# Kernel optimization log

Measured on AMD Instinct MI355X. Metric: run time of the kernel, lower is better.

The kernel has to match this reference:

```python
import jax, jax.numpy as jnp
import numpy as np

N_NODES = 100000

def _sage_conv(x, src, dst, Wl, bl, Wr, n_nodes):
    # PyG SAGEConv (mean aggr): out = lin_l(mean_{j in N(i)} x_j) + lin_r(x_i)
    msgs = x[src]                                            # [E, d] gather
    agg = jax.ops.segment_sum(msgs, dst, num_segments=n_nodes)   # [N, d]
    cnt = jax.ops.segment_sum(jnp.ones((src.shape[0],), x.dtype), dst,
                              num_segments=n_nodes)          # [N]
    mean = agg / jnp.maximum(cnt, 1.0)[:, None]              # mean aggregation
    return mean @ Wl.T + bl + x @ Wr.T

def setup_inputs() -> dict:
    key = jax.random.key(0)
    ks = jax.random.split(key, 6)
    d_in, d_hid, d_out = 64, 64, 2
    n_edges = 1600000
    x = jax.random.normal(ks[0], (N_NODES, d_in), dtype=jnp.float32)
    edge_index = jax.random.randint(ks[1], (2, n_edges), 0, N_NODES, dtype=jnp.int64)
    s = 1.0 / np.sqrt(d_in)
    W1l = jax.random.uniform(ks[2], (d_hid, d_in), jnp.float32, -s, s)
    b1l = jnp.zeros((d_hid,), jnp.float32)
    W1r = jax.random.uniform(ks[3], (d_hid, d_in), jnp.float32, -s, s)
    s2 = 1.0 / np.sqrt(d_hid)
    W2l = jax.random.uniform(ks[4], (d_out, d_hid), jnp.float32, -s2, s2)
    b2l = jnp.zeros((d_out,), jnp.float32)
    W2r = jax.random.uniform(ks[5], (d_out, d_hid), jnp.float32, -s2, s2)
    return {"x": x, "edge_index": edge_index, "W1l": W1l, "b1l": b1l,
            "W1r": W1r, "W2l": W2l, "b2l": b2l, "W2r": W2r}

def reference(x, edge_index, W1l, b1l, W1r, W2l, b2l, W2r):
    src, dst = edge_index[0], edge_index[1]
    h = _sage_conv(x, src, dst, W1l, b1l, W1r, N_NODES)
    h = jax.nn.relu(h)
    # F.dropout(p=0.5, training=False) is identity at inference
    out = _sage_conv(h, src, dst, W2l, b2l, W2r, N_NODES)
    return out
```

## Files before the change

### kernel.cpp

```cpp
#include <hip/hip_runtime.h>
#include <cstdint>

typedef long long i64;
typedef unsigned int u32;


#define BKT_SHIFT 8
#define BKT_MAX   512
#define BKT_CAP   5120
#define CHUNK     2048

__global__ __launch_bounds__(256) void k_detect(const int* __restrict__ e, int* __restrict__ flag) {
  __shared__ int nz;
  if (threadIdx.x == 0) nz = 0;
  __syncthreads();
  if (e[2 * threadIdx.x + 1] != 0) nz = 1;
  __syncthreads();
  if (threadIdx.x == 0) *flag = (nz == 0) ? 1 : 0;
}

__device__ __forceinline__ int edge_at(const void* eidx, int is64, size_t i) {
  return is64 ? (int)((const i64*)eidx)[i] : ((const int*)eidx)[i];
}

__global__ __launch_bounds__(256) void k_bucket(const void* __restrict__ eidx, const int* __restrict__ flag,
                                                int* __restrict__ gcount, u32* __restrict__ pairs, int E) {
  __shared__ int hist[BKT_MAX];
  __shared__ int basech[BKT_MAX];
  __shared__ int run[BKT_MAX];
  for (int i = threadIdx.x; i < BKT_MAX; i += 256) { hist[i] = 0; run[i] = 0; }
  __syncthreads();
  int is64 = *flag;
  int cbase = blockIdx.x * CHUNK;
  int cend = min(cbase + CHUNK, E);
  for (int e = cbase + threadIdx.x; e < cend; e += 256) {
    int d = edge_at(eidx, is64, (size_t)E + e);
    atomicAdd(&hist[d >> BKT_SHIFT], 1);
  }
  __syncthreads();
  for (int i = threadIdx.x; i < BKT_MAX; i += 256) {
    int h = hist[i];
    basech[i] = h ? (i * BKT_CAP + atomicAdd(&gcount[i], h)) : 0;
  }
  __syncthreads();
  for (int e = cbase + threadIdx.x; e < cend; e += 256) {
    int s = edge_at(eidx, is64, (size_t)e);
    int d = edge_at(eidx, is64, (size_t)E + e);
    int b = d >> BKT_SHIFT;
    int r = atomicAdd(&run[b], 1);
    pairs[basech[b] + r] = ((u32)s << 8) | (u32)(d & 255);
  }
}

__global__ __launch_bounds__(256) void k_csr(const int* __restrict__ gcount, const u32* __restrict__ pairs,
                                             int* __restrict__ csr_src, int* __restrict__ rs,
                                             int* __restrict__ re, int n_nodes) {
  __shared__ int cnt[256];
  __shared__ int sc[256];
  __shared__ int cur[256];
  int b = blockIdx.x, t = threadIdx.x;
  cnt[t] = 0;
  __syncthreads();
  int lo = b * BKT_CAP, hi = lo + gcount[b];
  for (int i = lo + t; i < hi; i += 256)
    atomicAdd(&cnt[pairs[i] & 255], 1);
  __syncthreads();
  int v = cnt[t];
  sc[t] = v;
  __syncthreads();
  for (int off = 1; off < 256; off <<= 1) {
    int a = (t >= off) ? sc[t - off] : 0;
    __syncthreads();
    sc[t] += a;
    __syncthreads();
  }
  int start = lo + sc[t] - v;
  int node = (b << BKT_SHIFT) + t;
  if (node < n_nodes) { rs[node] = start; re[node] = start + v; }
  cur[t] = start;
  __syncthreads();
  for (int i = lo + t; i < hi; i += 256) {
    u32 p = pairs[i];
    int q = atomicAdd(&cur[p & 255], 1);
    csr_src[q] = (int)(p >> 8);
  }
}

__global__ __launch_bounds__(256) void k_gemm1(const float* __restrict__ x,
                                               const float* __restrict__ Wl, const float* __restrict__ bl,
                                               const float* __restrict__ Wr,
                                               float* __restrict__ XL, float* __restrict__ XR, int n_nodes) {
  __shared__ float sWl[64 * 68];
  __shared__ float sWr[64 * 68];
  __shared__ float sX[64 * 68];
  int tid = threadIdx.x;
  int base = blockIdx.x * 64;

#pragma unroll
  for (int r = 0; r < 4; ++r) {
    int idx = tid + 256 * r;
    int f = idx >> 4, c4 = idx & 15;
    float4 wl = *(const float4*)(Wl + f * 64 + c4 * 4);
    float4 wr = *(const float4*)(Wr + f * 64 + c4 * 4);
    sWl[(c4 * 4 + 0) * 68 + f] = wl.x; sWl[(c4 * 4 + 1) * 68 + f] = wl.y;
    sWl[(c4 * 4 + 2) * 68 + f] = wl.z; sWl[(c4 * 4 + 3) * 68 + f] = wl.w;
    sWr[(c4 * 4 + 0) * 68 + f] = wr.x; sWr[(c4 * 4 + 1) * 68 + f] = wr.y;
    sWr[(c4 * 4 + 2) * 68 + f] = wr.z; sWr[(c4 * 4 + 3) * 68 + f] = wr.w;
  }
#pragma unroll
  for (int r = 0; r < 4; ++r) {
    int idx = tid + 256 * r;
    int nn = idx >> 4, c4 = idx & 15;
    int node = base + nn;
    float4 xv = make_float4(0.f, 0.f, 0.f, 0.f);
    if (node < n_nodes) xv = *(const float4*)(x + (size_t)node * 64 + c4 * 4);
    sX[(c4 * 4 + 0) * 68 + nn] = xv.x; sX[(c4 * 4 + 1) * 68 + nn] = xv.y;
    sX[(c4 * 4 + 2) * 68 + nn] = xv.z; sX[(c4 * 4 + 3) * 68 + nn] = xv.w;
  }
  __syncthreads();

  int f0 = (tid & 15) * 4, n0 = (tid >> 4) * 4;
  float accL[4][4] = {{0}}, accR[4][4] = {{0}};
#pragma unroll 8
  for (int k = 0; k < 64; ++k) {
    float4 xv = *(const float4*)&sX[k * 68 + n0];
    float4 wl = *(const float4*)&sWl[k * 68 + f0];
    float4 wr = *(const float4*)&sWr[k * 68 + f0];
    float xn[4] = {xv.x, xv.y, xv.z, xv.w};
    float wlf[4] = {wl.x, wl.y, wl.z, wl.w};
    float wrf[4] = {wr.x, wr.y, wr.z, wr.w};
#pragma unroll
    for (int a = 0; a < 4; ++a)
#pragma unroll
      for (int b = 0; b < 4; ++b) {
        accL[a][b] += xn[a] * wlf[b];
        accR[a][b] += xn[a] * wrf[b];
      }
  }

  float4 blv = *(const float4*)(bl + f0);
#pragma unroll
  for (int a = 0; a < 4; ++a) {
    int node = base + n0 + a;
    if (node >= n_nodes) continue;
    float4 ol = make_float4(accL[a][0], accL[a][1], accL[a][2], accL[a][3]);
    float4 orr = make_float4(accR[a][0] + blv.x, accR[a][1] + blv.y,
                             accR[a][2] + blv.z, accR[a][3] + blv.w);
    *(float4*)(XL + (size_t)node * 64 + f0) = ol;
    *(float4*)(XR + (size_t)node * 64 + f0) = orr;
  }
}

__global__ __launch_bounds__(256) void k_agg1g2(const int* __restrict__ rs, const int* __restrict__ re,
                                                const int* __restrict__ csr_src,
                                                const float* __restrict__ XL, const float* __restrict__ XR,
                                                const float* __restrict__ W2l, const float* __restrict__ b2l,
                                                const float* __restrict__ W2r,
                                                float* __restrict__ HL, float* __restrict__ HR,
                                                int n_nodes) {
  int wave = threadIdx.x >> 6, lane = threadIdx.x & 63;
  int g = lane >> 4, c = lane & 15;
  int n = (blockIdx.x * 4 + wave) * 4 + g;
  if (n >= n_nodes) return;

  float4 wl0 = *(const float4*)(W2l + c * 4);
  float4 wl1 = *(const float4*)(W2l + 64 + c * 4);
  float4 wr0 = *(const float4*)(W2r + c * 4);
  float4 wr1 = *(const float4*)(W2r + 64 + c * 4);
  float4 xr = *(const float4*)(XR + (size_t)n * 64 + c * 4);

  int start = rs[n], end = re[n];
  float4 a0 = make_float4(0.f, 0.f, 0.f, 0.f);
  float4 a1 = make_float4(0.f, 0.f, 0.f, 0.f);
  float4 a2 = make_float4(0.f, 0.f, 0.f, 0.f);
  float4 a3 = make_float4(0.f, 0.f, 0.f, 0.f);
  int e = start;
  for (; e + 3 < end; e += 4) {
    int s0 = csr_src[e], s1 = csr_src[e + 1], s2 = csr_src[e + 2], s3 = csr_src[e + 3];
    float4 v0 = *(const float4*)(XL + (size_t)s0 * 64 + c * 4);
    float4 v1 = *(const float4*)(XL + (size_t)s1 * 64 + c * 4);
    float4 v2 = *(const float4*)(XL + (size_t)s2 * 64 + c * 4);
    float4 v3 = *(const float4*)(XL + (size_t)s3 * 64 + c * 4);
    a0.x += v0.x; a0.y += v0.y; a0.z += v0.z; a0.w += v0.w;
    a1.x += v1.x; a1.y += v1.y; a1.z += v1.z; a1.w += v1.w;
    a2.x += v2.x; a2.y += v2.y; a2.z += v2.z; a2.w += v2.w;
    a3.x += v3.x; a3.y += v3.y; a3.z += v3.z; a3.w += v3.w;
  }
  if (e + 1 < end) {
    int s0 = csr_src[e], s1 = csr_src[e + 1];
    float4 v0 = *(const float4*)(XL + (size_t)s0 * 64 + c * 4);
    float4 v1 = *(const float4*)(XL + (size_t)s1 * 64 + c * 4);
    a0.x += v0.x; a0.y += v0.y; a0.z += v0.z; a0.w += v0.w;
    a1.x += v1.x; a1.y += v1.y; a1.z += v1.z; a1.w += v1.w;
    e += 2;
  }
  if (e < end) {
    int s0 = csr_src[e];
    float4 v0 = *(const float4*)(XL + (size_t)s0 * 64 + c * 4);
    a0.x += v0.x; a0.y += v0.y; a0.z += v0.z; a0.w += v0.w;
  }
  float inv = 1.0f / fmaxf((float)(end - start), 1.0f);
  float4 h;
  h.x = fmaxf((a0.x + a1.x + a2.x + a3.x) * inv + xr.x, 0.f);
  h.y = fmaxf((a0.y + a1.y + a2.y + a3.y) * inv + xr.y, 0.f);
  h.z = fmaxf((a0.z + a1.z + a2.z + a3.z) * inv + xr.z, 0.f);
  h.w = fmaxf((a0.w + a1.w + a2.w + a3.w) * inv + xr.w, 0.f);

  float p0 = h.x * wl0.x + h.y * wl0.y + h.z * wl0.z + h.w * wl0.w;
  float p1 = h.x * wl1.x + h.y * wl1.y + h.z * wl1.z + h.w * wl1.w;
  float q0 = h.x * wr0.x + h.y * wr0.y + h.z * wr0.z + h.w * wr0.w;
  float q1 = h.x * wr1.x + h.y * wr1.y + h.z * wr1.z + h.w * wr1.w;
#pragma unroll
  for (int off = 1; off < 16; off <<= 1) {
    p0 += __shfl_xor(p0, off, 16);
    p1 += __shfl_xor(p1, off, 16);
    q0 += __shfl_xor(q0, off, 16);
    q1 += __shfl_xor(q1, off, 16);
  }
  if (c == 0) {
    *(float2*)(HL + (size_t)n * 2) = make_float2(p0, p1);
    *(float2*)(HR + (size_t)n * 2) = make_float2(q0 + b2l[0], q1 + b2l[1]);
  }
}

__global__ __launch_bounds__(256) void k_agg2(const int* __restrict__ rs, const int* __restrict__ re,
                                              const int* __restrict__ csr_src,
                                              const float* __restrict__ HL, const float* __restrict__ HR,
                                              float* __restrict__ out, int n_nodes) {
  int n = blockIdx.x * 256 + threadIdx.x;
  if (n >= n_nodes) return;
  int start = rs[n], end = re[n];
  float s0 = 0.f, s1 = 0.f;
  int e = start;
  for (; e + 1 < end; e += 2) {
    int sa = csr_src[e], sb = csr_src[e + 1];
    float2 va = *(const float2*)(HL + (size_t)sa * 2);
    float2 vb = *(const float2*)(HL + (size_t)sb * 2);
    s0 += va.x + vb.x; s1 += va.y + vb.y;
  }
  if (e < end) {
    int sa = csr_src[e];
    float2 va = *(const float2*)(HL + (size_t)sa * 2);
    s0 += va.x; s1 += va.y;
  }
  float inv = 1.0f / fmaxf((float)(end - start), 1.0f);
  float2 hr = *(const float2*)(HR + (size_t)n * 2);
  out[n * 2 + 0] = s0 * inv + hr.x;
  out[n * 2 + 1] = s1 * inv + hr.y;
}

extern "C" void kernel_launch(void* const* d_in, const int* in_sizes, int n_in,
                              void* d_out, int out_size, void* d_ws, size_t ws_size,
                              hipStream_t stream) {
  const float* x   = (const float*)d_in[0];
  const void*  eix = d_in[1];
  const float* W1l = (const float*)d_in[2];
  const float* b1l = (const float*)d_in[3];
  const float* W1r = (const float*)d_in[4];
  const float* W2l = (const float*)d_in[5];
  const float* b2l = (const float*)d_in[6];
  const float* W2r = (const float*)d_in[7];
  float* out = (float*)d_out;

  const int N = in_sizes[0] / 64;
  const int E = in_sizes[1] / 2;
  const int NB = (N + 255) >> BKT_SHIFT;

  char* base = (char*)d_ws;
  size_t off = 0;
  auto alloc = [&](size_t bytes) {
    char* p = base + off;
    off = (off + bytes + 255) & ~(size_t)255;
    return p;
  };
  int*   gcount  = (int*)alloc((size_t)BKT_MAX * 4);
  int*   flag    = (int*)alloc(256);
  int*   rs      = (int*)alloc((size_t)N * 4);
  int*   re      = (int*)alloc((size_t)N * 4);
  int*   csr_src = (int*)alloc((size_t)NB * BKT_CAP * 4);
  float* XL      = (float*)alloc((size_t)N * 64 * 4);
  float* XR      = (float*)alloc((size_t)N * 64 * 4);
  float* HL      = (float*)alloc((size_t)N * 2 * 4);
  float* HR      = (float*)alloc((size_t)N * 2 * 4);
  u32*   pairs   = (u32*)XL;
  (void)ws_size;

  const int nb_bkt = (E + CHUNK - 1) / CHUNK;

  hipMemsetAsync(gcount, 0, (size_t)BKT_MAX * 4, stream);
  k_detect<<<1, 256, 0, stream>>>((const int*)eix, flag);
  k_bucket<<<nb_bkt, 256, 0, stream>>>(eix, flag, gcount, pairs, E);
  k_csr<<<NB, 256, 0, stream>>>(gcount, pairs, csr_src, rs, re, N);

  k_gemm1<<<(N + 63) / 64, 256, 0, stream>>>(x, W1l, b1l, W1r, XL, XR, N);
  k_agg1g2<<<(N + 15) / 16, 256, 0, stream>>>(rs, re, csr_src, XL, XR, W2l, b2l, W2r, HL, HR, N);
  k_agg2<<<(N + 255) / 256, 256, 0, stream>>>(rs, re, csr_src, HL, HR, out, N);
}
```

Baseline: 232.3 us.

## Fuse edge bucketing with first GEMM and vectorize CSR build

Merges the dtype detection, edge bucketing and first-layer GEMM into one launch, with block ranges split between the two jobs so they can run concurrently. This needs a separate pairs buffer instead of aliasing XL. The CSR build kernel now uses 512 threads and uint4 loads of the packed pairs, and the aggregation loop gains an 8-way unrolled gather. Each bucketing block recomputes the int64 detection, and the fused kernel's larger shared-memory footprint applies to the bucketing blocks too, which may lower their occupancy.

```diff
diff --git a/kernel.cpp b/kernel.cpp
--- a/kernel.cpp
+++ b/kernel.cpp
@@ -10,91 +10,63 @@
 #define BKT_CAP   5120
 #define CHUNK     2048
 
-__global__ __launch_bounds__(256) void k_detect(const int* __restrict__ e, int* __restrict__ flag) {
-  __shared__ int nz;
-  if (threadIdx.x == 0) nz = 0;
-  __syncthreads();
-  if (e[2 * threadIdx.x + 1] != 0) nz = 1;
-  __syncthreads();
-  if (threadIdx.x == 0) *flag = (nz == 0) ? 1 : 0;
-}
-
 __device__ __forceinline__ int edge_at(const void* eidx, int is64, size_t i) {
   return is64 ? (int)((const i64*)eidx)[i] : ((const int*)eidx)[i];
 }
 
-__global__ __launch_bounds__(256) void k_bucket(const void* __restrict__ eidx, const int* __restrict__ flag,
-                                                int* __restrict__ gcount, u32* __restrict__ pairs, int E) {
-  __shared__ int hist[BKT_MAX];
-  __shared__ int basech[BKT_MAX];
-  __shared__ int run[BKT_MAX];
-  for (int i = threadIdx.x; i < BKT_MAX; i += 256) { hist[i] = 0; run[i] = 0; }
-  __syncthreads();
-  int is64 = *flag;
-  int cbase = blockIdx.x * CHUNK;
-  int cend = min(cbase + CHUNK, E);
-  for (int e = cbase + threadIdx.x; e < cend; e += 256) {
-    int d = edge_at(eidx, is64, (size_t)E + e);
-    atomicAdd(&hist[d >> BKT_SHIFT], 1);
-  }
-  __syncthreads();
-  for (int i = threadIdx.x; i < BKT_MAX; i += 256) {
-    int h = hist[i];
-    basech[i] = h ? (i * BKT_CAP + atomicAdd(&gcount[i], h)) : 0;
-  }
-  __syncthreads();
-  for (int e = cbase + threadIdx.x; e < cend; e += 256) {
-    int s = edge_at(eidx, is64, (size_t)e);
-    int d = edge_at(eidx, is64, (size_t)E + e);
-    int b = d >> BKT_SHIFT;
-    int r = atomicAdd(&run[b], 1);
-    pairs[basech[b] + r] = ((u32)s << 8) | (u32)(d & 255);
-  }
-}
-
-__global__ __launch_bounds__(256) void k_csr(const int* __restrict__ gcount, const u32* __restrict__ pairs,
-                                             int* __restrict__ csr_src, int* __restrict__ rs,
-                                             int* __restrict__ re, int n_nodes) {
-  __shared__ int cnt[256];
-  __shared__ int sc[256];
-  __shared__ int cur[256];
-  int b = blockIdx.x, t = threadIdx.x;
-  cnt[t] = 0;
-  __syncthreads();
-  int lo = b * BKT_CAP, hi = lo + gcount[b];
-  for (int i = lo + t; i < hi; i += 256)
-    atomicAdd(&cnt[pairs[i] & 255], 1);
-  __syncthreads();
-  int v = cnt[t];
-  sc[t] = v;
-  __syncthreads();
-  for (int off = 1; off < 256; off <<= 1) {
-    int a = (t >= off) ? sc[t - off] : 0;
-    __syncthreads();
-    sc[t] += a;
-    __syncthreads();
-  }
-  int start = lo + sc[t] - v;
-  int node = (b << BKT_SHIFT) + t;
-  if (node < n_nodes) { rs[node] = start; re[node] = start + v; }
-  cur[t] = start;
-  __syncthreads();
-  for (int i = lo + t; i < hi; i += 256) {
-    u32 p = pairs[i];
-    int q = atomicAdd(&cur[p & 255], 1);
-    csr_src[q] = (int)(p >> 8);
-  }
-}
-
-__global__ __launch_bounds__(256) void k_gemm1(const float* __restrict__ x,
-                                               const float* __restrict__ Wl, const float* __restrict__ bl,
-                                               const float* __restrict__ Wr,
-                                               float* __restrict__ XL, float* __restrict__ XR, int n_nodes) {
-  __shared__ float sWl[64 * 68];
-  __shared__ float sWr[64 * 68];
-  __shared__ float sX[64 * 68];
+__global__ __launch_bounds__(256) void k_pre(const void* __restrict__ eidx,
+                                             int* __restrict__ gcount, u32* __restrict__ pairs, int E,
+                                             const float* __restrict__ x,
+                                             const float* __restrict__ Wl, const float* __restrict__ bl,
+                                             const float* __restrict__ Wr,
+                                             float* __restrict__ XL, float* __restrict__ XR,
+                                             int n_nodes, int nbkt) {
+  __shared__ float smem[64 * 68 * 3];
   int tid = threadIdx.x;
-  int base = blockIdx.x * 64;
+
+  if ((int)blockIdx.x < nbkt) {
+    int* hist   = (int*)smem;
+    int* basech = hist + BKT_MAX;
+    int* run    = basech + BKT_MAX;
+    int* nzp    = run + BKT_MAX;
+    for (int i = tid; i < BKT_MAX; i += 256) { hist[i] = 0; run[i] = 0; }
+    if (tid == 0) *nzp = 0;
+    __syncthreads();
+    if (((const int*)eidx)[2 * tid + 1] != 0) *nzp = 1;
+    __syncthreads();
+    int is64 = (*nzp == 0);
+
+    int cbase = blockIdx.x * CHUNK;
+    int sreg[8], dreg[8];
+#pragma unroll
+    for (int i = 0; i < 8; ++i) {
+      int e = cbase + tid + 256 * i;
+      bool v = e < E;
+      sreg[i] = v ? edge_at(eidx, is64, (size_t)e) : 0;
+      dreg[i] = v ? edge_at(eidx, is64, (size_t)E + e) : -1;
+      if (v) atomicAdd(&hist[dreg[i] >> BKT_SHIFT], 1);
+    }
+    __syncthreads();
+    for (int i = tid; i < BKT_MAX; i += 256) {
+      int h = hist[i];
+      basech[i] = h ? (i * BKT_CAP + atomicAdd(&gcount[i], h)) : 0;
+    }
+    __syncthreads();
+#pragma unroll
+    for (int i = 0; i < 8; ++i) {
+      if (dreg[i] >= 0) {
+        int b = dreg[i] >> BKT_SHIFT;
+        int r = atomicAdd(&run[b], 1);
+        pairs[basech[b] + r] = ((u32)sreg[i] << 8) | (u32)(dreg[i] & 255);
+      }
+    }
+    return;
+  }
+
+  float* sWl = smem;
+  float* sWr = smem + 64 * 68;
+  float* sX  = smem + 2 * 64 * 68;
+  int base = (blockIdx.x - nbkt) * 64;
 
 #pragma unroll
   for (int r = 0; r < 4; ++r) {
@@ -148,6 +120,54 @@
                              accR[a][2] + blv.z, accR[a][3] + blv.w);
     *(float4*)(XL + (size_t)node * 64 + f0) = ol;
     *(float4*)(XR + (size_t)node * 64 + f0) = orr;
+  }
+}
+
+__global__ __launch_bounds__(512) void k_csr(const int* __restrict__ gcount, const u32* __restrict__ pairs,
+                                             int* __restrict__ csr_src, int* __restrict__ rs,
+                                             int* __restrict__ re, int n_nodes) {
+  __shared__ int cnt[256];
+  __shared__ int sc[256];
+  __shared__ int cur[256];
+  int b = blockIdx.x, t = threadIdx.x;
+  if (t < 256) cnt[t] = 0;
+  __syncthreads();
+  int n = gcount[b];
+  int lo = b * BKT_CAP, hi = lo + n;
+  int tail = n & 3;
+  for (int i = lo + t * 4; i + 3 < hi; i += 2048) {
+    uint4 p = *(const uint4*)(pairs + i);
+    atomicAdd(&cnt[p.x & 255], 1); atomicAdd(&cnt[p.y & 255], 1);
+    atomicAdd(&cnt[p.z & 255], 1); atomicAdd(&cnt[p.w & 255], 1);
+  }
+  if (t < tail) atomicAdd(&cnt[pairs[hi - tail + t] & 255], 1);
+  __syncthreads();
+  int v = (t < 256) ? cnt[t] : 0;
+  if (t < 256) sc[t] = v;
+  __syncthreads();
+  for (int off = 1; off < 256; off <<= 1) {
+    int a = (t >= off && t < 256) ? sc[t - off] : 0;
+    __syncthreads();
+    if (t < 256) sc[t] += a;
+    __syncthreads();
+  }
+  if (t < 256) {
+    int start = lo + sc[t] - v;
+    int node = (b << BKT_SHIFT) + t;
+    if (node < n_nodes) { rs[node] = start; re[node] = start + v; }
+    cur[t] = start;
+  }
+  __syncthreads();
+  for (int i = lo + t * 4; i + 3 < hi; i += 2048) {
+    uint4 p = *(const uint4*)(pairs + i);
+    csr_src[atomicAdd(&cur[p.x & 255], 1)] = (int)(p.x >> 8);
+    csr_src[atomicAdd(&cur[p.y & 255], 1)] = (int)(p.y >> 8);
+    csr_src[atomicAdd(&cur[p.z & 255], 1)] = (int)(p.z >> 8);
+    csr_src[atomicAdd(&cur[p.w & 255], 1)] = (int)(p.w >> 8);
+  }
+  if (t < tail) {
+    u32 p = pairs[hi - tail + t];
+    csr_src[atomicAdd(&cur[p & 255], 1)] = (int)(p >> 8);
   }
 }
 
@@ -175,6 +195,26 @@
   float4 a2 = make_float4(0.f, 0.f, 0.f, 0.f);
   float4 a3 = make_float4(0.f, 0.f, 0.f, 0.f);
   int e = start;
+  for (; e + 7 < end; e += 8) {
+    int s0 = csr_src[e],     s1 = csr_src[e + 1], s2 = csr_src[e + 2], s3 = csr_src[e + 3];
+    int s4 = csr_src[e + 4], s5 = csr_src[e + 5], s6 = csr_src[e + 6], s7 = csr_src[e + 7];
+    float4 v0 = *(const float4*)(XL + (size_t)s0 * 64 + c * 4);
+    float4 v1 = *(const float4*)(XL + (size_t)s1 * 64 + c * 4);
+    float4 v2 = *(const float4*)(XL + (size_t)s2 * 64 + c * 4);
+    float4 v3 = *(const float4*)(XL + (size_t)s3 * 64 + c * 4);
+    float4 v4 = *(const float4*)(XL + (size_t)s4 * 64 + c * 4);
+    float4 v5 = *(const float4*)(XL + (size_t)s5 * 64 + c * 4);
+    float4 v6 = *(const float4*)(XL + (size_t)s6 * 64 + c * 4);
+    float4 v7 = *(const float4*)(XL + (size_t)s7 * 64 + c * 4);
+    a0.x += v0.x; a0.y += v0.y; a0.z += v0.z; a0.w += v0.w;
+    a1.x += v1.x; a1.y += v1.y; a1.z += v1.z; a1.w += v1.w;
+    a2.x += v2.x; a2.y += v2.y; a2.z += v2.z; a2.w += v2.w;
+    a3.x += v3.x; a3.y += v3.y; a3.z += v3.z; a3.w += v3.w;
+    a0.x += v4.x; a0.y += v4.y; a0.z += v4.z; a0.w += v4.w;
+    a1.x += v5.x; a1.y += v5.y; a1.z += v5.z; a1.w += v5.w;
+    a2.x += v6.x; a2.y += v6.y; a2.z += v6.z; a2.w += v6.w;
+    a3.x += v7.x; a3.y += v7.y; a3.z += v7.z; a3.w += v7.w;
+  }
   for (; e + 3 < end; e += 4) {
     int s0 = csr_src[e], s1 = csr_src[e + 1], s2 = csr_src[e + 2], s3 = csr_src[e + 3];
     float4 v0 = *(const float4*)(XL + (size_t)s0 * 64 + c * 4);
@@ -274,25 +314,23 @@
     return p;
   };
   int*   gcount  = (int*)alloc((size_t)BKT_MAX * 4);
-  int*   flag    = (int*)alloc(256);
   int*   rs      = (int*)alloc((size_t)N * 4);
   int*   re      = (int*)alloc((size_t)N * 4);
   int*   csr_src = (int*)alloc((size_t)NB * BKT_CAP * 4);
+  u32*   pairs   = (u32*)alloc((size_t)NB * BKT_CAP * 4);
   float* XL      = (float*)alloc((size_t)N * 64 * 4);
   float* XR      = (float*)alloc((size_t)N * 64 * 4);
   float* HL      = (float*)alloc((size_t)N * 2 * 4);
   float* HR      = (float*)alloc((size_t)N * 2 * 4);
-  u32*   pairs   = (u32*)XL;
   (void)ws_size;
 
-  const int nb_bkt = (E + CHUNK - 1) / CHUNK;
+  const int nbkt = (E + CHUNK - 1) / CHUNK;
+  const int ngem = (N + 63) / 64;
 
   hipMemsetAsync(gcount, 0, (size_t)BKT_MAX * 4, stream);
-  k_detect<<<1, 256, 0, stream>>>((const int*)eix, flag);
-  k_bucket<<<nb_bkt, 256, 0, stream>>>(eix, flag, gcount, pairs, E);
-  k_csr<<<NB, 256, 0, stream>>>(gcount, pairs, csr_src, rs, re, N);
-
-  k_gemm1<<<(N + 63) / 64, 256, 0, stream>>>(x, W1l, b1l, W1r, XL, XR, N);
+  k_pre<<<nbkt + ngem, 256, 0, stream>>>(eix, gcount, pairs, E,
+                                         x, W1l, b1l, W1r, XL, XR, N, nbkt);
+  k_csr<<<NB, 512, 0, stream>>>(gcount, pairs, csr_src, rs, re, N);
   k_agg1g2<<<(N + 15) / 16, 256, 0, stream>>>(rs, re, csr_src, XL, XR, W2l, b2l, W2r, HL, HR, N);
   k_agg2<<<(N + 255) / 256, 256, 0, stream>>>(rs, re, csr_src, HL, HR, out, N);
 }
```

After: 219.4 us. 5.6% less time.
